# Kernel tuning notes

Hardware: AMD Instinct MI355X
Metric: run time of the kernel (lower is better)

## Reference

```python
import jax, jax.numpy as jnp
import numpy as np

N_EMBD = 1024
N_HEAD = 16
HEAD_DIM = N_EMBD // N_HEAD
D_FF = 4 * N_EMBD
B, T = 2, 2048


def setup_inputs() -> dict:
    key = jax.random.key(0)
    ks = jax.random.split(key, 16)
    s = 0.02
    d = {
        'x': jax.random.normal(ks[0], (B, T, N_EMBD), jnp.float32),
        'ln1_g': jnp.ones((N_EMBD,), jnp.float32),
        'ln1_b': jnp.zeros((N_EMBD,), jnp.float32),
        'Wq': jax.random.normal(ks[1], (N_EMBD, N_EMBD), jnp.float32) * s,
        'bq': jnp.zeros((N_EMBD,), jnp.float32),
        'Wk': jax.random.normal(ks[2], (N_EMBD, N_EMBD), jnp.float32) * s,
        'bk': jnp.zeros((N_EMBD,), jnp.float32),
        'Wv': jax.random.normal(ks[3], (N_EMBD, N_EMBD), jnp.float32) * s,
        'bv': jnp.zeros((N_EMBD,), jnp.float32),
        'Wo': jax.random.normal(ks[4], (N_EMBD, N_EMBD), jnp.float32) * s,
        'bo': jnp.zeros((N_EMBD,), jnp.float32),
        'ln2_g': jnp.ones((N_EMBD,), jnp.float32),
        'ln2_b': jnp.zeros((N_EMBD,), jnp.float32),
        'W1': jax.random.normal(ks[5], (N_EMBD, D_FF), jnp.float32) * s,
        'b1': jnp.zeros((D_FF,), jnp.float32),
        'W2': jax.random.normal(ks[6], (D_FF, N_EMBD), jnp.float32) * s,
        'b2': jnp.zeros((N_EMBD,), jnp.float32),
    }
    return d


def _layernorm(x, g, b, eps=1e-5):
    mu = jnp.mean(x, axis=-1, keepdims=True)
    var = jnp.var(x, axis=-1, keepdims=True)
    return (x - mu) * jax.lax.rsqrt(var + eps) * g + b


def _attention(x, Wq, bq, Wk, bk, Wv, bv, Wo, bo):
    b, t, c = x.shape
    q = (x @ Wq + bq).reshape(b, t, N_HEAD, HEAD_DIM).transpose(0, 2, 1, 3)
    k = (x @ Wk + bk).reshape(b, t, N_HEAD, HEAD_DIM).transpose(0, 2, 1, 3)
    v = (x @ Wv + bv).reshape(b, t, N_HEAD, HEAD_DIM).transpose(0, 2, 1, 3)
    att = jnp.einsum('bhqd,bhkd->bhqk', q, k) / jnp.sqrt(jnp.float32(HEAD_DIM))
    causal = jnp.tril(jnp.ones((t, t), bool))
    att = jnp.where(causal[None, None], att, -jnp.inf)
    att = jax.nn.softmax(att, axis=-1)
    y = jnp.einsum('bhqk,bhkd->bhqd', att, v)
    y = y.transpose(0, 2, 1, 3).reshape(b, t, c)
    return y @ Wo + bo


def reference(x, ln1_g, ln1_b, Wq, bq, Wk, bk, Wv, bv, Wo, bo, ln2_g, ln2_b, W1, b1, W2, b2):
    x = x + _attention(_layernorm(x, ln1_g, ln1_b), Wq, bq, Wk, bk, Wv, bv, Wo, bo)
    h = _layernorm(x, ln2_g, ln2_b)
    h = jax.nn.gelu(h @ W1 + b1, approximate=False) @ W2 + b2
    return x + h
```

## Files before the change

kernel.cpp:

```cpp
#include <hip/hip_runtime.h>
#include <hip/hip_bf16.h>

typedef __hip_bfloat16 bf16;
using bf16x8 = __attribute__((ext_vector_type(8))) short;
using f32x4  = __attribute__((ext_vector_type(4))) float;
using f32x16 = __attribute__((ext_vector_type(16))) float;
using u32x4  = __attribute__((ext_vector_type(4))) unsigned int;

#define TSEQ 2048
#define NH   16
#define HD   64
#define NC   1024
#define DFF  4096
#define NROWS 4096

__device__ __forceinline__ void load_lds16(const bf16* g, bf16* l) {
  __builtin_amdgcn_global_load_lds(
      (const __attribute__((address_space(1))) unsigned int*)g,
      (__attribute__((address_space(3))) unsigned int*)l, 16, 0, 0);
}

__device__ __forceinline__ float b2f(short s) {
  unsigned int u = ((unsigned int)(unsigned short)s) << 16;
  return __builtin_bit_cast(float, u);
}

__device__ __forceinline__ unsigned cvtpk(float a, float b) {
  unsigned r;
  asm("v_cvt_pk_bf16_f32 %0, %1, %2" : "=v"(r) : "v"(a), "v"(b));
  return r;
}

__device__ __forceinline__ void pl32swap(unsigned &d, unsigned &s) {
  asm("v_permlane32_swap_b32 %0, %1" : "+v"(d), "+v"(s));
}

__device__ __forceinline__ float gelu_f(float x) {
  float u = 0.7978845608028654f * fmaf(0.044715f * x, x * x, x);
  float e = __expf(2.0f * u);
  float t = 1.0f - 2.0f / (e + 1.0f);
  return 0.5f * x * (1.0f + t);
}

__global__ __launch_bounds__(256)
void ln_cast_kernel(const float* __restrict__ x, const float* __restrict__ g,
                    const float* __restrict__ b, bf16* __restrict__ out) {
  int row = blockIdx.x, tid = threadIdx.x;
  const float4 v = ((const float4*)(x + (size_t)row * NC))[tid];
  float s  = v.x + v.y + v.z + v.w;
  float s2 = v.x*v.x + v.y*v.y + v.z*v.z + v.w*v.w;
#pragma unroll
  for (int m = 1; m < 64; m <<= 1) { s += __shfl_xor(s, m); s2 += __shfl_xor(s2, m); }
  __shared__ float rs[4], rs2[4];
  if ((tid & 63) == 0) { rs[tid >> 6] = s; rs2[tid >> 6] = s2; }
  __syncthreads();
  s  = rs[0] + rs[1] + rs[2] + rs[3];
  s2 = rs2[0] + rs2[1] + rs2[2] + rs2[3];
  float mu   = s * (1.0f / NC);
  float var  = s2 * (1.0f / NC) - mu * mu;
  float rstd = rsqrtf(var + 1e-5f);
  const float4 gv = ((const float4*)g)[tid];
  const float4 bv = ((const float4*)b)[tid];
  bf16* o = out + (size_t)row * NC + tid * 4;
  o[0] = __float2bfloat16((v.x - mu) * rstd * gv.x + bv.x);
  o[1] = __float2bfloat16((v.y - mu) * rstd * gv.y + bv.y);
  o[2] = __float2bfloat16((v.z - mu) * rstd * gv.z + bv.z);
  o[3] = __float2bfloat16((v.w - mu) * rstd * gv.w + bv.w);
}

__global__ __launch_bounds__(256)
void wo_ln_kernel(const float* __restrict__ x, const float* __restrict__ bo,
                  const bf16* __restrict__ P, const float* __restrict__ g,
                  const float* __restrict__ bln, float* __restrict__ x2,
                  bf16* __restrict__ xn2) {
  int row = blockIdx.x, tid = threadIdx.x;
  size_t base = (size_t)row * NC + tid * 4;
  const float4 xv = *(const float4*)(x + base);
  const float4 bv = ((const float4*)bo)[tid];
  short4 p0 = *(const short4*)((const short*)P + base);
  short4 p1 = *(const short4*)((const short*)P + (size_t)NROWS * NC + base);
  float v0 = xv.x + bv.x + b2f(p0.x) + b2f(p1.x);
  float v1 = xv.y + bv.y + b2f(p0.y) + b2f(p1.y);
  float v2 = xv.z + bv.z + b2f(p0.z) + b2f(p1.z);
  float v3 = xv.w + bv.w + b2f(p0.w) + b2f(p1.w);
  float4 ov = {v0, v1, v2, v3};
  *(float4*)(x2 + base) = ov;
  float s  = v0 + v1 + v2 + v3;
  float s2 = v0*v0 + v1*v1 + v2*v2 + v3*v3;
#pragma unroll
  for (int m = 1; m < 64; m <<= 1) { s += __shfl_xor(s, m); s2 += __shfl_xor(s2, m); }
  __shared__ float rs[4], rs2[4];
  if ((tid & 63) == 0) { rs[tid >> 6] = s; rs2[tid >> 6] = s2; }
  __syncthreads();
  s  = rs[0] + rs[1] + rs[2] + rs[3];
  s2 = rs2[0] + rs2[1] + rs2[2] + rs2[3];
  float mu   = s * (1.0f / NC);
  float var  = s2 * (1.0f / NC) - mu * mu;
  float rstd = rsqrtf(var + 1e-5f);
  const float4 gv = ((const float4*)g)[tid];
  const float4 lv = ((const float4*)bln)[tid];
  bf16* o = xn2 + base;
  o[0] = __float2bfloat16((v0 - mu) * rstd * gv.x + lv.x);
  o[1] = __float2bfloat16((v1 - mu) * rstd * gv.y + lv.y);
  o[2] = __float2bfloat16((v2 - mu) * rstd * gv.z + lv.z);
  o[3] = __float2bfloat16((v3 - mu) * rstd * gv.w + lv.w);
}

__global__ __launch_bounds__(256)
void w2_final_kernel(const float* __restrict__ x2, const float* __restrict__ b2,
                     const bf16* __restrict__ P, float* __restrict__ out) {
  int row = blockIdx.x, tid = threadIdx.x;
  size_t base = (size_t)row * NC + tid * 4;
  const float4 xv = *(const float4*)(x2 + base);
  const float4 bv = ((const float4*)b2)[tid];
  float a0 = xv.x + bv.x, a1 = xv.y + bv.y, a2 = xv.z + bv.z, a3 = xv.w + bv.w;
#pragma unroll
  for (int z = 0; z < 4; ++z) {
    short4 p = *(const short4*)((const short*)P + (size_t)z * NROWS * NC + base);
    a0 += b2f(p.x); a1 += b2f(p.y); a2 += b2f(p.z); a3 += b2f(p.w);
  }
  float4 ov = {a0, a1, a2, a3};
  *(float4*)(out + base) = ov;
}

__global__ __launch_bounds__(256)
void transpose_all_kernel(const float* __restrict__ Wq, const float* __restrict__ Wk,
                          const float* __restrict__ Wv, const float* __restrict__ Wo,
                          const float* __restrict__ W1, const float* __restrict__ W2,
                          bf16* __restrict__ WqkvoT, bf16* __restrict__ W1T,
                          bf16* __restrict__ W2T) {
  int bid = blockIdx.x;
  const float* W; bf16* Wt; int K, N, nx, tile;
  if (bid < 4096) {
    int z = bid >> 10; tile = bid & 1023;
    W = (z == 0) ? Wq : (z == 1) ? Wk : (z == 2) ? Wv : Wo;
    Wt = WqkvoT + (size_t)z * NC * NC; K = NC; N = NC; nx = 32;
  } else if (bid < 8192) {
    tile = bid - 4096; W = W1; Wt = W1T; K = NC; N = DFF; nx = 128;
  } else {
    tile = bid - 8192; W = W2; Wt = W2T; K = DFF; N = NC; nx = 32;
  }
  int n0 = (tile % nx) * 32, k0 = (tile / nx) * 32;
  __shared__ float t[32][33];
  int tx = threadIdx.x, ty = threadIdx.y;
#pragma unroll
  for (int i = 0; i < 4; ++i)
    t[ty + i * 8][tx] = W[(size_t)(k0 + ty + i * 8) * N + n0 + tx];
  __syncthreads();
#pragma unroll
  for (int i = 0; i < 4; ++i)
    Wt[(size_t)(n0 + ty + i * 8) * K + k0 + tx] = __float2bfloat16(t[tx][ty + i * 8]);
}

#define MODE_GELU 4
#define MODE_QKV  5
#define MODE_PART 6

template <int MODE>
__global__ __launch_bounds__(256)
void gemm_bt(const bf16* __restrict__ A, const bf16* __restrict__ Bt,
             const float* __restrict__ bias, const float* __restrict__ bias2,
             const float* __restrict__ bias3,
             void* __restrict__ outp, void* __restrict__ out2, void* __restrict__ out3,
             int M, int N, int K, int KS) {
  __shared__ bf16 As[128 * 64];
  __shared__ bf16 Bs[128 * 64];
  int tid  = threadIdx.x;
  int w    = tid >> 6;
  int lane = tid & 63;
  int l32  = lane & 31;
  int khalf = lane >> 5;
  int sx   = lane & 7;
  int waveM = (w >> 1) * 64, waveN = (w & 1) * 64;

  int gN = gridDim.x, gM = gridDim.y;
  int pid = blockIdx.y * gN + blockIdx.x;
  int npg = 8 * gN;
  int gid = pid / npg;
  int fm  = gid * 8;
  int gsz = min(gM - fm, 8);
  int bm = (fm + (pid % gsz)) * 128;
  int bn = ((pid % npg) / gsz) * 128;

  int k_beg = blockIdx.z * KS;

  const bf16* pA[4]; const bf16* pB[4];
#pragma unroll
  for (int i = 0; i < 4; ++i) {
    int p = i * 256 + tid;
    int row = p >> 3;
    int lc = (p & 7) ^ (row & 7);
    pA[i] = A  + (size_t)(bm + row) * K + k_beg + lc * 8;
    pB[i] = Bt + (size_t)(bn + row) * K + k_beg + lc * 8;
  }

  f32x16 acc[2][2];
#pragma unroll
  for (int mi = 0; mi < 2; ++mi)
#pragma unroll
    for (int ni = 0; ni < 2; ++ni)
#pragma unroll
      for (int r = 0; r < 16; ++r) acc[mi][ni][r] = 0.f;

  for (int kt = 0; kt < KS; kt += 64) {
    __syncthreads();
#pragma unroll
    for (int i = 0; i < 4; ++i) {
      load_lds16(pA[i], &As[(i * 256 + w * 64) * 8]);
      load_lds16(pB[i], &Bs[(i * 256 + w * 64) * 8]);
      pA[i] += 64; pB[i] += 64;
    }
    __syncthreads();
#pragma unroll
    for (int s = 0; s < 4; ++s) {
      int ch = ((s * 2 + khalf) ^ sx) * 8;
      bf16x8 af[2], bfr[2];
#pragma unroll
      for (int mi = 0; mi < 2; ++mi)
        af[mi] = *(const bf16x8*)&As[(waveM + mi * 32 + l32) * 64 + ch];
#pragma unroll
      for (int ni = 0; ni < 2; ++ni)
        bfr[ni] = *(const bf16x8*)&Bs[(waveN + ni * 32 + l32) * 64 + ch];
#pragma unroll
      for (int mi = 0; mi < 2; ++mi)
#pragma unroll
        for (int ni = 0; ni < 2; ++ni)
          acc[mi][ni] = __builtin_amdgcn_mfma_f32_32x32x16_bf16(af[mi], bfr[ni], acc[mi][ni], 0, 0, 0);
    }
  }

  if (MODE == MODE_PART) {
    bf16* dst = (bf16*)outp + (size_t)blockIdx.z * M * N;
#pragma unroll
    for (int mi = 0; mi < 2; ++mi)
#pragma unroll
      for (int ni = 0; ni < 2; ++ni) {
        int col = bn + waveN + ni * 32 + l32;
#pragma unroll
        for (int reg = 0; reg < 16; ++reg) {
          int row = bm + waveM + mi * 32 + (reg & 3) + 8 * (reg >> 2) + 4 * khalf;
          dst[(size_t)row * N + col] = __float2bfloat16(acc[mi][ni][reg]);
        }
      }
  } else if (MODE == MODE_GELU) {
    float bcol[2];
#pragma unroll
    for (int ni = 0; ni < 2; ++ni) bcol[ni] = bias[bn + waveN + ni * 32 + l32];
#pragma unroll
    for (int mi = 0; mi < 2; ++mi)
#pragma unroll
      for (int ni = 0; ni < 2; ++ni) {
        int col = bn + waveN + ni * 32 + l32;
#pragma unroll
        for (int reg = 0; reg < 16; ++reg) {
          int row = bm + waveM + mi * 32 + (reg & 3) + 8 * (reg >> 2) + 4 * khalf;
          ((bf16*)outp)[(size_t)row * N + col] =
              __float2bfloat16(gelu_f(acc[mi][ni][reg] + bcol[ni]));
        }
      }
  } else {
    int seg = bn >> 10;
    int c1b = (bn & (NC - 1)) + waveN;
    const float* bp = (seg == 0) ? bias : (seg == 1) ? bias2 : bias3;
    float bcol[2]; int hh[2], dd[2];
#pragma unroll
    for (int ni = 0; ni < 2; ++ni) {
      int c1 = c1b + ni * 32 + l32;
      bcol[ni] = bp[c1]; hh[ni] = c1 >> 6; dd[ni] = c1 & (HD - 1);
    }
    if (seg < 2) {
      bf16* dst = (seg == 0) ? (bf16*)outp : (bf16*)out2;
#pragma unroll
      for (int mi = 0; mi < 2; ++mi)
#pragma unroll
        for (int reg = 0; reg < 16; ++reg) {
          int row = bm + waveM + mi * 32 + (reg & 3) + 8 * (reg >> 2) + 4 * khalf;
          int bbi = row >> 11, t = row & (TSEQ - 1);
#pragma unroll
          for (int ni = 0; ni < 2; ++ni)
            dst[((size_t)(bbi * NH + hh[ni]) * TSEQ + t) * HD + dd[ni]] =
                __float2bfloat16(acc[mi][ni][reg] + bcol[ni]);
        }
    } else {
      bf16* dst = (bf16*)out3;
#pragma unroll
      for (int mi = 0; mi < 2; ++mi)
#pragma unroll
        for (int reg = 0; reg < 16; ++reg) {
          int row = bm + waveM + mi * 32 + (reg & 3) + 8 * (reg >> 2) + 4 * khalf;
          int bbi = row >> 11, t = row & (TSEQ - 1);
#pragma unroll
          for (int ni = 0; ni < 2; ++ni)
            dst[((size_t)(bbi * NH + hh[ni]) * HD + dd[ni]) * TSEQ + t] =
                __float2bfloat16(acc[mi][ni][reg] + bcol[ni]);
        }
    }
  }
}

__global__ __launch_bounds__(64)
void attn_kernel(const bf16* __restrict__ q, const bf16* __restrict__ k,
                 const bf16* __restrict__ vT, bf16* __restrict__ out) {
  int id   = blockIdx.x;
  int xcd  = id & 7;
  int slot = id >> 3;
  int bh   = xcd * 4 + (slot >> 6);
  int s64  = slot & 63;
  int qt   = (s64 < 32) ? (2 * s64) : (63 - 2 * (s64 - 32));
  int b = bh >> 4, h = bh & 15;

  int lane = threadIdx.x;
  int l31  = lane & 31;
  int hh   = lane >> 5;
  int h8   = hh * 8;
  int base4 = hh * 4;

  const bf16* qp = q  + (size_t)(b * NH + h) * TSEQ * HD;
  const bf16* kp = k  + (size_t)(b * NH + h) * TSEQ * HD;
  const bf16* vp = vT + (size_t)(b * NH + h) * HD * TSEQ;

  int q0 = qt * 32;

  bf16x8 qf[4];
#pragma unroll
  for (int ds = 0; ds < 4; ++ds)
    qf[ds] = *(const bf16x8*)(qp + (size_t)(q0 + l31) * HD + ds * 16 + h8);

  f32x16 o0, o1;
#pragma unroll
  for (int r = 0; r < 16; ++r) { o0[r] = 0.f; o1[r] = 0.f; }
  float lacc = 0.f;

  const bf16* kb = kp + (size_t)l31 * HD + h8;
  const bf16* vb = vp + (size_t)l31 * TSEQ + h8;

  bf16x8 a0 = *(const bf16x8*)(kb);
  bf16x8 a1 = *(const bf16x8*)(kb + 16);
  bf16x8 a2 = *(const bf16x8*)(kb + 32);
  bf16x8 a3 = *(const bf16x8*)(kb + 48);

  auto step = [&](int kt, bool dg) {
    int k0 = kt * 32;
    bf16x8 v00 = *(const bf16x8*)(vb + k0);
    bf16x8 v01 = *(const bf16x8*)(vb + k0 + 16);
    bf16x8 v10 = *(const bf16x8*)(vb + (size_t)32 * TSEQ + k0);
    bf16x8 v11 = *(const bf16x8*)(vb + (size_t)32 * TSEQ + k0 + 16);
    bf16x8 n0, n1, n2, n3;
    if (!dg) {
      const bf16* kn = kb + (size_t)(k0 + 32) * HD;
      n0 = *(const bf16x8*)(kn);
      n1 = *(const bf16x8*)(kn + 16);
      n2 = *(const bf16x8*)(kn + 32);
      n3 = *(const bf16x8*)(kn + 48);
    }

    f32x16 c;
#pragma unroll
    for (int r = 0; r < 16; ++r) c[r] = 0.f;
    c = __builtin_amdgcn_mfma_f32_32x32x16_bf16(a0, qf[0], c, 0, 0, 0);
    c = __builtin_amdgcn_mfma_f32_32x32x16_bf16(a1, qf[1], c, 0, 0, 0);
    c = __builtin_amdgcn_mfma_f32_32x32x16_bf16(a2, qf[2], c, 0, 0, 0);
    c = __builtin_amdgcn_mfma_f32_32x32x16_bf16(a3, qf[3], c, 0, 0, 0);

    float p[16];
    float ls = 0.f;
#pragma unroll
    for (int r = 0; r < 16; ++r) {
      float pv = exp2f(fmaf(c[r], 0.18033688011112042f, -11.541560327111707f));
      if (dg) {
        int krr = (r & 3) + 8 * (r >> 2) + base4;
        pv = (krr <= l31) ? pv : 0.f;
      }
      p[r] = pv;
      ls += pv;
    }
    lacc += ls;

    unsigned A0 = cvtpk(p[0],  p[1]),  C0 = cvtpk(p[4],  p[5]);
    unsigned B0 = cvtpk(p[2],  p[3]),  D0 = cvtpk(p[6],  p[7]);
    pl32swap(A0, C0); pl32swap(B0, D0);
    unsigned A1 = cvtpk(p[8],  p[9]),  C1 = cvtpk(p[12], p[13]);
    unsigned B1 = cvtpk(p[10], p[11]), D1 = cvtpk(p[14], p[15]);
    pl32swap(A1, C1); pl32swap(B1, D1);
    u32x4 w0 = {A0, B0, C0, D0};
    u32x4 w1 = {A1, B1, C1, D1};
    bf16x8 pa0 = __builtin_bit_cast(bf16x8, w0);
    bf16x8 pa1 = __builtin_bit_cast(bf16x8, w1);

    o0 = __builtin_amdgcn_mfma_f32_32x32x16_bf16(pa0, v00, o0, 0, 0, 0);
    o0 = __builtin_amdgcn_mfma_f32_32x32x16_bf16(pa1, v01, o0, 0, 0, 0);
    o1 = __builtin_amdgcn_mfma_f32_32x32x16_bf16(pa0, v10, o1, 0, 0, 0);
    o1 = __builtin_amdgcn_mfma_f32_32x32x16_bf16(pa1, v11, o1, 0, 0, 0);

    if (!dg) { a0 = n0; a1 = n1; a2 = n2; a3 = n3; }
  };

  for (int kt = 0; kt < qt; ++kt) step(kt, false);
  step(qt, true);

  float ltot = lacc + __shfl_xor(lacc, 32);
  float linv = 1.0f / ltot;
#pragma unroll
  for (int r = 0; r < 16; ++r) {
    int qoff = (r & 3) + 8 * (r >> 2) + base4;
    float sc = __shfl(linv, qoff);
    size_t ob = ((size_t)(b * TSEQ + q0 + qoff)) * NC + h * HD + l31;
    out[ob]      = __float2bfloat16(o0[r] * sc);
    out[ob + 32] = __float2bfloat16(o1[r] * sc);
  }
}

extern "C" void kernel_launch(void* const* d_in, const int* in_sizes, int n_in,
                              void* d_out, int out_size, void* d_ws, size_t ws_size,
                              hipStream_t stream) {
  const float* x     = (const float*)d_in[0];
  const float* ln1_g = (const float*)d_in[1];
  const float* ln1_b = (const float*)d_in[2];
  const float* Wq    = (const float*)d_in[3];
  const float* bq    = (const float*)d_in[4];
  const float* Wk    = (const float*)d_in[5];
  const float* bk    = (const float*)d_in[6];
  const float* Wv    = (const float*)d_in[7];
  const float* bv    = (const float*)d_in[8];
  const float* Wo    = (const float*)d_in[9];
  const float* bo    = (const float*)d_in[10];
  const float* ln2_g = (const float*)d_in[11];
  const float* ln2_b = (const float*)d_in[12];
  const float* W1    = (const float*)d_in[13];
  const float* b1    = (const float*)d_in[14];
  const float* W2    = (const float*)d_in[15];
  const float* b2    = (const float*)d_in[16];

  char* ws = (char*)d_ws;
  const size_t MB = 1u << 20;
  bf16* WqkvT = (bf16*)(ws + 0 * MB);
  bf16* W1T  = (bf16*)(ws + 8 * MB);
  bf16* W2T  = (bf16*)(ws + 16 * MB);
  bf16* xn1  = (bf16*)(ws + 24 * MB);
  bf16* qb   = (bf16*)(ws + 32 * MB);
  bf16* kb   = (bf16*)(ws + 40 * MB);
  bf16* vTb  = (bf16*)(ws + 48 * MB);
  bf16* att  = (bf16*)(ws + 56 * MB);
  float* x2  = (float*)(ws + 64 * MB);
  bf16* xn2  = (bf16*)(ws + 80 * MB);
  bf16* h1   = (bf16*)(ws + 88 * MB);
  bf16* woP  = (bf16*)(ws + 88 * MB);
  bf16* w2P  = (bf16*)(ws + 32 * MB);
  bf16* WoT  = WqkvT + 3 * (size_t)NC * NC;

  transpose_all_kernel<<<12288, dim3(32, 8), 0, stream>>>(
      Wq, Wk, Wv, Wo, W1, W2, WqkvT, W1T, W2T);

  ln_cast_kernel<<<NROWS, 256, 0, stream>>>(x, ln1_g, ln1_b, xn1);

  gemm_bt<MODE_QKV><<<dim3(24, 32, 1), 256, 0, stream>>>(
      xn1, WqkvT, bq, bk, bv, qb, kb, vTb, NROWS, 3 * NC, NC, NC);

  attn_kernel<<<2048, 64, 0, stream>>>(qb, kb, vTb, att);

  gemm_bt<MODE_PART><<<dim3(8, 32, 2), 256, 0, stream>>>(
      att, WoT, nullptr, nullptr, nullptr, woP, nullptr, nullptr, NROWS, NC, NC, NC / 2);

  wo_ln_kernel<<<NROWS, 256, 0, stream>>>(x, bo, woP, ln2_g, ln2_b, x2, xn2);

  gemm_bt<MODE_GELU><<<dim3(32, 32, 1), 256, 0, stream>>>(
      xn2, W1T, b1, nullptr, nullptr, h1, nullptr, nullptr, NROWS, DFF, NC, NC);

  gemm_bt<MODE_PART><<<dim3(8, 32, 4), 256, 0, stream>>>(
      h1, W2T, nullptr, nullptr, nullptr, w2P, nullptr, nullptr, NROWS, NC, DFF, DFF / 4);

  w2_final_kernel<<<NROWS, 256, 0, stream>>>(x2, b2, w2P, (float*)d_out);
}
```

Measured before the change: 372.6 us.

## Split attention key loop across four waves with LDS reduction

After: 370.9 us. No clear change (-0.4%).

```diff
diff --git a/kernel.cpp b/kernel.cpp
--- a/kernel.cpp
+++ b/kernel.cpp
@@ -298,18 +298,20 @@
   }
 }
 
-__global__ __launch_bounds__(64)
+__global__ __launch_bounds__(256)
 void attn_kernel(const bf16* __restrict__ q, const bf16* __restrict__ k,
                  const bf16* __restrict__ vT, bf16* __restrict__ out) {
-  int id   = blockIdx.x;
-  int xcd  = id & 7;
-  int slot = id >> 3;
-  int bh   = xcd * 4 + (slot >> 6);
-  int s64  = slot & 63;
-  int qt   = (s64 < 32) ? (2 * s64) : (63 - 2 * (s64 - 32));
+  int id  = blockIdx.x;
+  int xcd = id & 7;
+  int t   = id >> 3;
+  int bh  = xcd * 4 + (t & 3);
+  int u   = t >> 2;
+  int qt  = (u < 32) ? (2 * u) : (63 - 2 * (u - 32));
   int b = bh >> 4, h = bh & 15;
 
-  int lane = threadIdx.x;
+  int tid  = threadIdx.x;
+  int w    = tid >> 6;
+  int lane = tid & 63;
   int l31  = lane & 31;
   int hh   = lane >> 5;
   int h8   = hh * 8;
@@ -334,10 +336,7 @@
   const bf16* kb = kp + (size_t)l31 * HD + h8;
   const bf16* vb = vp + (size_t)l31 * TSEQ + h8;
 
-  bf16x8 a0 = *(const bf16x8*)(kb);
-  bf16x8 a1 = *(const bf16x8*)(kb + 16);
-  bf16x8 a2 = *(const bf16x8*)(kb + 32);
-  bf16x8 a3 = *(const bf16x8*)(kb + 48);
+  bf16x8 a0, a1, a2, a3;
 
   auto step = [&](int kt, bool dg) {
     int k0 = kt * 32;
@@ -346,8 +345,9 @@
     bf16x8 v10 = *(const bf16x8*)(vb + (size_t)32 * TSEQ + k0);
     bf16x8 v11 = *(const bf16x8*)(vb + (size_t)32 * TSEQ + k0 + 16);
     bf16x8 n0, n1, n2, n3;
-    if (!dg) {
-      const bf16* kn = kb + (size_t)(k0 + 32) * HD;
+    bool pf = !dg && (kt + 4 <= qt);
+    if (pf) {
+      const bf16* kn = kb + (size_t)(k0 + 128) * HD;
       n0 = *(const bf16x8*)(kn);
       n1 = *(const bf16x8*)(kn + 16);
       n2 = *(const bf16x8*)(kn + 32);
@@ -382,31 +382,63 @@
     unsigned A1 = cvtpk(p[8],  p[9]),  C1 = cvtpk(p[12], p[13]);
     unsigned B1 = cvtpk(p[10], p[11]), D1 = cvtpk(p[14], p[15]);
     pl32swap(A1, C1); pl32swap(B1, D1);
-    u32x4 w0 = {A0, B0, C0, D0};
-    u32x4 w1 = {A1, B1, C1, D1};
-    bf16x8 pa0 = __builtin_bit_cast(bf16x8, w0);
-    bf16x8 pa1 = __builtin_bit_cast(bf16x8, w1);
+    u32x4 w0v = {A0, B0, C0, D0};
+    u32x4 w1v = {A1, B1, C1, D1};
+    bf16x8 pa0 = __builtin_bit_cast(bf16x8, w0v);
+    bf16x8 pa1 = __builtin_bit_cast(bf16x8, w1v);
 
     o0 = __builtin_amdgcn_mfma_f32_32x32x16_bf16(pa0, v00, o0, 0, 0, 0);
     o0 = __builtin_amdgcn_mfma_f32_32x32x16_bf16(pa1, v01, o0, 0, 0, 0);
     o1 = __builtin_amdgcn_mfma_f32_32x32x16_bf16(pa0, v10, o1, 0, 0, 0);
     o1 = __builtin_amdgcn_mfma_f32_32x32x16_bf16(pa1, v11, o1, 0, 0, 0);
 
-    if (!dg) { a0 = n0; a1 = n1; a2 = n2; a3 = n3; }
+    if (pf) { a0 = n0; a1 = n1; a2 = n2; a3 = n3; }
   };
 
-  for (int kt = 0; kt < qt; ++kt) step(kt, false);
-  step(qt, true);
-
-  float ltot = lacc + __shfl_xor(lacc, 32);
-  float linv = 1.0f / ltot;
-#pragma unroll
-  for (int r = 0; r < 16; ++r) {
-    int qoff = (r & 3) + 8 * (r >> 2) + base4;
-    float sc = __shfl(linv, qoff);
-    size_t ob = ((size_t)(b * TSEQ + q0 + qoff)) * NC + h * HD + l31;
-    out[ob]      = __float2bfloat16(o0[r] * sc);
-    out[ob + 32] = __float2bfloat16(o1[r] * sc);
+  if (w <= qt) {
+    const bf16* ka = kb + (size_t)w * 32 * HD;
+    a0 = *(const bf16x8*)(ka);
+    a1 = *(const bf16x8*)(ka + 16);
+    a2 = *(const bf16x8*)(ka + 32);
+    a3 = *(const bf16x8*)(ka + 48);
+    int diag = (w == (qt & 3)) ? 1 : 0;
+    int T = ((qt - w) >> 2) + 1 - diag;
+    int kt = w;
+    for (int i = 0; i < T; ++i, kt += 4) step(kt, false);
+    if (diag) step(qt, true);
+  }
+
+  __shared__ float red[2][64][33];
+  auto dump = [&](int slot) {
+    float* d = &red[slot][lane][0];
+#pragma unroll
+    for (int r = 0; r < 16; ++r) { d[r] = o0[r]; d[16 + r] = o1[r]; }
+    d[32] = lacc;
+  };
+  auto gather = [&](int slot) {
+    const float* s = &red[slot][lane][0];
+#pragma unroll
+    for (int r = 0; r < 16; ++r) { o0[r] += s[r]; o1[r] += s[16 + r]; }
+    lacc += s[32];
+  };
+  if (w >= 2) dump(w - 2);
+  __syncthreads();
+  if (w < 2) gather(w);
+  __syncthreads();
+  if (w == 1) dump(0);
+  __syncthreads();
+  if (w == 0) {
+    gather(0);
+    float ltot = lacc + __shfl_xor(lacc, 32);
+    float linv = 1.0f / ltot;
+#pragma unroll
+    for (int r = 0; r < 16; ++r) {
+      int qoff = (r & 3) + 8 * (r >> 2) + base4;
+      float sc = __shfl(linv, qoff);
+      size_t ob = ((size_t)(b * TSEQ + q0 + qoff)) * NC + h * HD + l31;
+      out[ob]      = __float2bfloat16(o0[r] * sc);
+      out[ob + 32] = __float2bfloat16(o1[r] * sc);
+    }
   }
 }
 
@@ -456,7 +488,7 @@
   gemm_bt<MODE_QKV><<<dim3(24, 32, 1), 256, 0, stream>>>(
       xn1, WqkvT, bq, bk, bv, qb, kb, vTb, NROWS, 3 * NC, NC, NC);
 
-  attn_kernel<<<2048, 64, 0, stream>>>(qb, kb, vTb, att);
+  attn_kernel<<<2048, 256, 0, stream>>>(qb, kb, vTb, att);
 
   gemm_bt<MODE_PART><<<dim3(8, 32, 2), 256, 0, stream>>>(
       att, WoT, nullptr, nullptr, nullptr, woP, nullptr, nullptr, NROWS, NC, NC, NC / 2);
```
